# Optimization experiments

Hardware: AMD Instinct MI355X
Metric: run time of the kernel (lower is better)

Reference implementation:

```python
import jax, jax.numpy as jnp
import numpy as np

T = 2048
N = 4096
DT = 0.01
V_RESET = 1.0
ALPHA = 0.01
MAX_SPIKES = 128


def setup_inputs() -> dict:
    key = jax.random.key(0)
    ks = jax.random.split(key, 8)
    ts = jnp.arange(T, dtype=jnp.float32) * DT
    input_current = jax.random.normal(ks[0], (T, N), dtype=jnp.float32)
    # _build_w: uniform(minval=0.5) fully-connected weight matrix
    w = jax.random.uniform(ks[1], (N, N), dtype=jnp.float32, minval=0.5, maxval=1.0)
    # _build_initial: uniform(maxval=0.1)
    v0 = jax.random.uniform(ks[2], (N,), dtype=jnp.float32, maxval=0.1)
    i0 = jax.random.uniform(ks[3], (N,), dtype=jnp.float32, maxval=0.1)
    mu = jax.random.uniform(ks[4], (2,), dtype=jnp.float32, minval=0.5, maxval=1.0)
    # uniforms for initial s and for post-spike s resampling (s = log(u) - alpha)
    s0_u = jax.random.uniform(ks[5], (N,), dtype=jnp.float32)
    resample_u = jax.random.uniform(ks[6], (T, N), dtype=jnp.float32)
    return {"ts": ts, "input_current": input_current, "w": w, "v0": v0,
            "i0": i0, "mu": mu, "s0_u": s0_u, "resample_u": resample_u,
            "max_spikes": MAX_SPIKES}


def reference(ts, input_current, w, v0, i0, mu, s0_u, resample_u, max_spikes):
    """Event-driven spiking net: Euler integration of the drift vf with
    spike events when s crosses 0, followed by the masked per-neuron jump
    transition (_inner_trans_fn) using the firing neuron's weight row.
    Returns trajectory ys [T, N, 3] (v, i, s per neuron)."""
    dt = ts[1] - ts[0]
    eps = jnp.float32(1e-12)
    # s0 = log(uniform) - alpha  (always negative; drifts up at rate intensity(v))
    s0 = jnp.log(s0_u + eps) - ALPHA
    y0 = jnp.stack([v0, i0, s0], axis=-1)  # [N, 3]
    mu1, mu2 = mu[0], mu[1]

    def step(carry, xs):
        y, nsp = carry
        inp_t, ru_t = xs
        v, i, s = y[:, 0], y[:, 1], y[:, 2]
        # drift_vf (Euler step)
        v_n = v + dt * (mu1 * (i - v) + mu1 * inp_t)
        i_n = i + dt * (-mu2 * i)
        s_n = s + dt * jax.nn.sigmoid(v)  # intensity_fn(v)
        # event detection: cond_fn = s; event when s reaches 0
        ev = s_n >= 0.0  # [N] event mask
        fire = jnp.any(ev) & (nsp < max_spikes)
        idx = jnp.argmax(ev)  # event_idx = argmax over event mask
        w_row = w[idx]  # weights from firing neuron to all neurons
        # _inner_trans_fn: spiking neurons reset v and resample s;
        # non-spiking neurons receive current injection w[idx][j]
        v_t = jnp.where(ev, v_n - V_RESET, v_n)
        i_t = jnp.where(ev, i_n, i_n + w_row)
        s_t = jnp.where(ev, jnp.log(ru_t + eps) - ALPHA, s_n)
        y_fire = jnp.stack([v_t, i_t, s_t], axis=-1)
        y_free = jnp.stack([v_n, i_n, s_n], axis=-1)
        y_out = jnp.where(fire, y_fire, y_free)
        nsp = nsp + fire.astype(jnp.int32)
        return (y_out, nsp), y_out

    (_, _), ys = jax.lax.scan(step, (y0, jnp.int32(0)),
                              (input_current, resample_u))
    return ys
```

## Files before the change

### kernel.cpp

```cpp
#include <hip/hip_runtime.h>
#include <stddef.h>

#define TT 2048
#define NN 4096
#define LSEG 64
#define NSEG (TT / LSEG)
#define NBLK 16
#define TPB 256
#define MAXU 0xFFFFFFFFu
#define NOFIRE 0xFFFFFFFEu

__global__ __launch_bounds__(TPB) void phaseA(
    const float* __restrict__ ts, const float* __restrict__ inp,
    const float* __restrict__ w, const float* __restrict__ v0,
    const float* __restrict__ i0, const float* __restrict__ mu,
    const float* __restrict__ s0u, const float* __restrict__ ru,
    const int* __restrict__ mx, float* __restrict__ ys,
    unsigned int* __restrict__ hdr, unsigned int* __restrict__ slots)
{
#pragma clang fp contract(off)
  const int tid = threadIdx.x;
  const int n = blockIdx.x * TPB + tid;
  const float dt = ts[1] - ts[0];
  const float mu1 = mu[0], mu2 = mu[1];
  const int maxs = mx[0];

  float v = v0[n];
  float i_nw = i0[n];
  float s = logf(s0u[n] + 1e-12f) - 0.01f;
  float wv = 0.0f;
  bool applyw = false;
  float inpv = inp[n];
  float ruv  = ru[n];
  int nsp = 0;
  int t_stop = TT;

  __shared__ unsigned int sh_w[TPB / 64];
  __shared__ unsigned int sh_b;

  for (int t = 0; t < TT; ++t) {
    float inpv_n = 0.0f, ruv_n = 0.0f;
    if (t + 1 < TT) {
      inpv_n = inp[(size_t)(t + 1) * NN + n];
      ruv_n  = ru[(size_t)(t + 1) * NN + n];
    }
    float logru = logf(ruv + 1e-12f) - 0.01f;
    float sig = 1.0f / (1.0f + expf(-v));
    float sn = s + dt * sig;
    bool ev = sn >= 0.0f;
    bool coupled = (nsp < maxs);

    if (coupled) {
      unsigned int m = ev ? (unsigned int)n : NOFIRE;
#pragma unroll
      for (int off = 32; off > 0; off >>= 1) {
        unsigned int o = (unsigned int)__shfl_down((int)m, off, 64);
        m = m < o ? m : o;
      }
      if ((tid & 63) == 0) sh_w[tid >> 6] = m;
      __syncthreads();
      if (tid == 0) {
        unsigned int bm = sh_w[0];
        for (int k = 1; k < TPB / 64; ++k) bm = bm < sh_w[k] ? bm : sh_w[k];
        __hip_atomic_store(&slots[(size_t)t * NBLK + blockIdx.x], bm,
                           __ATOMIC_RELAXED, __HIP_MEMORY_SCOPE_AGENT);
      }
    }

    float i_full = applyw ? (i_nw + wv) : i_nw;
    if (t > 0) {
      size_t o = ((size_t)(t - 1) * NN + n) * 3;
      ys[o] = v; ys[o + 1] = i_full; ys[o + 2] = s;
    }
    float vn  = v + dt * (mu1 * (i_full - v) + mu1 * inpv);
    float in_ = i_full + dt * (-mu2 * i_full);

    unsigned int gm = NOFIRE;
    if (coupled) {
      if (tid == 0) {
        unsigned int res = NOFIRE;
        long guard = 0;
        for (;;) {
          unsigned int mn = MAXU;
          bool all = true;
#pragma unroll
          for (int bk = 0; bk < NBLK; ++bk) {
            unsigned int x = __hip_atomic_load(&slots[(size_t)t * NBLK + bk],
                                               __ATOMIC_RELAXED,
                                               __HIP_MEMORY_SCOPE_AGENT);
            all = all && (x != MAXU);
            mn = mn < x ? mn : x;
          }
          if (all || ++guard > (1L << 21)) { res = mn; break; }
        }
        sh_b = res;
      }
      __syncthreads();
      gm = sh_b;
    }

    bool fire = coupled && (gm < (unsigned int)NN);
    applyw = false;
    if (fire) {
      nsp += 1;
      wv = w[(size_t)gm * NN + n];
      if (ev) { v = vn - 1.0f; s = logru; }
      else    { v = vn; s = sn; applyw = true; }
    } else {
      v = vn; s = sn;
    }
    i_nw = in_;
    inpv = inpv_n; ruv = ruv_n;

    if (nsp >= maxs && ((t + 1) & (LSEG - 1)) == 0) { t_stop = t + 1; break; }
  }

  {
    float i_full = applyw ? (i_nw + wv) : i_nw;
    size_t o = ((size_t)(t_stop - 1) * NN + n) * 3;
    ys[o] = v; ys[o + 1] = i_full; ys[o + 2] = s;
  }
  if (n == 0) hdr[0] = (unsigned int)t_stop;
}

__global__ __launch_bounds__(TPB) void p1_segc(
    const float* __restrict__ ts, const float* __restrict__ inp,
    const float* __restrict__ mu, const float* __restrict__ ys,
    const unsigned int* __restrict__ hdr, float* __restrict__ buf1)
{
  unsigned int Kp = hdr[0];
  unsigned int g0 = Kp / LSEG;
  unsigned int g = blockIdx.x >> 4;
  if (g < g0) return;
  int n = (blockIdx.x & 15) * TPB + threadIdx.x;
  float dt = ts[1] - ts[0];
  float mu1 = mu[0], mu2 = mu[1];
  float a = 1.0f - dt * mu1, b = dt * mu1, r = 1.0f - dt * mu2;
  float ibase = ys[((size_t)(Kp - 1) * NN + n) * 3 + 1];
  float ij = ibase * powf(r, (float)((int)(g * LSEG) - (int)Kp));
  float c = 0.0f;
  size_t base = (size_t)(g * LSEG) * NN + n;
  for (int j = 0; j < LSEG; ++j) {
    float x = inp[base + (size_t)j * NN];
    c = a * c + b * (ij + x);
    ij *= r;
  }
  buf1[(size_t)g * NN + n] = c;
}

__global__ __launch_bounds__(TPB) void p2_scanv(
    const float* __restrict__ ts, const float* __restrict__ mu,
    const float* __restrict__ ys, const unsigned int* __restrict__ hdr,
    float* __restrict__ buf1)
{
  unsigned int Kp = hdr[0];
  unsigned int g0 = Kp / LSEG;
  if (g0 >= NSEG) return;
  int n = blockIdx.x * TPB + threadIdx.x;
  float dt = ts[1] - ts[0];
  float mu1 = mu[0];
  float a = 1.0f - dt * mu1;
  float aL = a;
  for (int k = 0; k < 6; ++k) aL *= aL;
  float v = ys[((size_t)(Kp - 1) * NN + n) * 3 + 0];
  for (unsigned int g = g0; g < NSEG; ++g) {
    float cg = buf1[(size_t)g * NN + n];
    buf1[(size_t)g * NN + n] = v;
    v = aL * v + cg;
  }
}

__global__ __launch_bounds__(TPB) void p3_seg(
    const float* __restrict__ ts, const float* __restrict__ inp,
    const float* __restrict__ mu, const unsigned int* __restrict__ hdr,
    const float* __restrict__ buf1, float* __restrict__ buf2,
    float* __restrict__ ys)
{
  unsigned int Kp = hdr[0];
  unsigned int g0 = Kp / LSEG;
  unsigned int g = blockIdx.x >> 4;
  if (g < g0) return;
  int n = (blockIdx.x & 15) * TPB + threadIdx.x;
  float dt = ts[1] - ts[0];
  float mu1 = mu[0], mu2 = mu[1];
  float r = 1.0f - dt * mu2;
  float v = buf1[(size_t)g * NN + n];
  float ibase = ys[((size_t)(Kp - 1) * NN + n) * 3 + 1];
  float i = ibase * powf(r, (float)((int)(g * LSEG) - (int)Kp));
  float sl = 0.0f;
  for (int j = 0; j < LSEG; ++j) {
    size_t t = (size_t)g * LSEG + j;
    float x = inp[t * NN + n];
    float sig = 1.0f / (1.0f + expf(-v));
    sl = sl + dt * sig;
    float vn  = v + dt * (mu1 * (i - v) + mu1 * x);
    float in_ = i + dt * (-mu2 * i);
    size_t o = (t * NN + n) * 3;
    ys[o] = vn; ys[o + 1] = in_; ys[o + 2] = sl;
    v = vn; i = in_;
  }
  buf2[(size_t)g * NN + n] = sl;
}

__global__ __launch_bounds__(TPB) void p4_scans(
    const float* __restrict__ ys, const unsigned int* __restrict__ hdr,
    float* __restrict__ buf2)
{
  unsigned int Kp = hdr[0];
  unsigned int g0 = Kp / LSEG;
  if (g0 >= NSEG) return;
  int n = blockIdx.x * TPB + threadIdx.x;
  float s = ys[((size_t)(Kp - 1) * NN + n) * 3 + 2];
  for (unsigned int g = g0; g < NSEG; ++g) {
    float t = buf2[(size_t)g * NN + n];
    buf2[(size_t)g * NN + n] = s;
    s += t;
  }
}

__global__ __launch_bounds__(TPB) void p5_fixs(
    const unsigned int* __restrict__ hdr, const float* __restrict__ buf2,
    float* __restrict__ ys)
{
  unsigned int Kp = hdr[0];
  size_t e = (size_t)Kp * NN + (size_t)blockIdx.x * TPB + threadIdx.x;
  if (e >= (size_t)TT * NN) return;
  unsigned int t = (unsigned int)(e >> 12);
  unsigned int n = (unsigned int)(e & (NN - 1));
  unsigned int g = t >> 6;
  ys[e * 3 + 2] += buf2[(size_t)g * NN + n];
}

extern "C" void kernel_launch(void* const* d_in, const int* in_sizes, int n_in,
                              void* d_out, int out_size, void* d_ws, size_t ws_size,
                              hipStream_t stream)
{
  (void)in_sizes; (void)n_in; (void)out_size; (void)ws_size;
  const float* ts  = (const float*)d_in[0];
  const float* inp = (const float*)d_in[1];
  const float* w   = (const float*)d_in[2];
  const float* v0  = (const float*)d_in[3];
  const float* i0  = (const float*)d_in[4];
  const float* mu  = (const float*)d_in[5];
  const float* s0u = (const float*)d_in[6];
  const float* ru  = (const float*)d_in[7];
  const int*   mx  = (const int*)d_in[8];
  float* ys = (float*)d_out;

  char* wsb = (char*)d_ws;
  unsigned int* hdr   = (unsigned int*)wsb;
  unsigned int* slots = (unsigned int*)(wsb + 1024);
  float* buf1 = (float*)(wsb + 1024 + (size_t)TT * NBLK * 4);
  float* buf2 = buf1 + (size_t)NSEG * NN;

  hipMemsetAsync(slots, 0xFF, (size_t)TT * NBLK * 4, stream);

  phaseA<<<NBLK, TPB, 0, stream>>>(ts, inp, w, v0, i0, mu, s0u, ru, mx, ys, hdr, slots);
  p1_segc<<<NSEG * 16, TPB, 0, stream>>>(ts, inp, mu, ys, hdr, buf1);
  p2_scanv<<<NN / TPB, TPB, 0, stream>>>(ts, mu, ys, hdr, buf1);
  p3_seg<<<NSEG * 16, TPB, 0, stream>>>(ts, inp, mu, hdr, buf1, buf2, ys);
  p4_scans<<<NN / TPB, TPB, 0, stream>>>(ys, hdr, buf2);
  p5_fixs<<<(TT - 128) * NN / TPB, TPB, 0, stream>>>(hdr, buf2, ys);
}
```

Before: 567.3 us.

## Replicate full neuron state per block to drop inter-block spin sync; fuse s fixup

Phase A no longer splits neurons across blocks that meet through global atomic slots every step. Each of 16 blocks of 1024 threads now simulates all 4096 neurons redundantly, 4 per thread, so the firing argmin comes from an intra-block shuffle and shared-memory reduction. Each block writes only its own quarter-slice of one 256-neuron chunk. The trailing phase also drops the separate s-fixup pass: a sigma-only pass produces segment sums and a final pass recomputes the trajectory and writes ys once with the scanned s offset. The trade is 16x redundant compute and input reads in phase A and one extra recompute pass, in exchange for removing the cross-block spin waits and one read-modify-write sweep of ys.

```diff
diff --git a/kernel.cpp b/kernel.cpp
--- a/kernel.cpp
+++ b/kernel.cpp
@@ -5,122 +5,135 @@
 #define NN 4096
 #define LSEG 64
 #define NSEG (TT / LSEG)
-#define NBLK 16
+#define ABLK 16
+#define ATPB 1024
+#define NPT 4
 #define TPB 256
-#define MAXU 0xFFFFFFFFu
 #define NOFIRE 0xFFFFFFFEu
 
-__global__ __launch_bounds__(TPB) void phaseA(
+__global__ __launch_bounds__(ATPB) void phaseA(
     const float* __restrict__ ts, const float* __restrict__ inp,
     const float* __restrict__ w, const float* __restrict__ v0,
     const float* __restrict__ i0, const float* __restrict__ mu,
     const float* __restrict__ s0u, const float* __restrict__ ru,
     const int* __restrict__ mx, float* __restrict__ ys,
-    unsigned int* __restrict__ hdr, unsigned int* __restrict__ slots)
+    unsigned int* __restrict__ hdr)
 {
 #pragma clang fp contract(off)
   const int tid = threadIdx.x;
-  const int n = blockIdx.x * TPB + tid;
+  const int bid = blockIdx.x;
   const float dt = ts[1] - ts[0];
   const float mu1 = mu[0], mu2 = mu[1];
   const int maxs = mx[0];
 
-  float v = v0[n];
-  float i_nw = i0[n];
-  float s = logf(s0u[n] + 1e-12f) - 0.01f;
-  float wv = 0.0f;
-  bool applyw = false;
-  float inpv = inp[n];
-  float ruv  = ru[n];
-  int nsp = 0;
-  int t_stop = TT;
-
-  __shared__ unsigned int sh_w[TPB / 64];
-  __shared__ unsigned int sh_b;
+  const int kw = bid >> 2;
+  const bool wr = ((tid >> 8) == (bid & 3));
+  const int nw = bid * 256 + (tid & 255);
+
+  float v[NPT], ci[NPT], s[NPT], wv[NPT], inpv[NPT], ruv[NPT];
+  bool aw[NPT];
+#pragma unroll
+  for (int k = 0; k < NPT; ++k) {
+    int n = tid + k * ATPB;
+    v[k] = v0[n];
+    ci[k] = i0[n];
+    s[k] = logf(s0u[n] + 1e-12f) - 0.01f;
+    wv[k] = 0.0f; aw[k] = false;
+    inpv[k] = inp[n];
+    ruv[k]  = ru[n];
+  }
+  int nsp = 0, t_stop = TT;
+
+  __shared__ unsigned int sh_w[2][ATPB / 64];
 
   for (int t = 0; t < TT; ++t) {
-    float inpv_n = 0.0f, ruv_n = 0.0f;
+    float inpn[NPT], run[NPT];
     if (t + 1 < TT) {
-      inpv_n = inp[(size_t)(t + 1) * NN + n];
-      ruv_n  = ru[(size_t)(t + 1) * NN + n];
-    }
-    float logru = logf(ruv + 1e-12f) - 0.01f;
-    float sig = 1.0f / (1.0f + expf(-v));
-    float sn = s + dt * sig;
-    bool ev = sn >= 0.0f;
+#pragma unroll
+      for (int k = 0; k < NPT; ++k) {
+        size_t o = (size_t)(t + 1) * NN + tid + k * ATPB;
+        inpn[k] = inp[o]; run[k] = ru[o];
+      }
+    } else {
+#pragma unroll
+      for (int k = 0; k < NPT; ++k) { inpn[k] = 0.0f; run[k] = 0.0f; }
+    }
+
+    float sn[NPT]; bool ev[NPT];
+    unsigned int m = NOFIRE;
+#pragma unroll
+    for (int k = 0; k < NPT; ++k) {
+      float sig = 1.0f / (1.0f + expf(-v[k]));
+      sn[k] = s[k] + dt * sig;
+      ev[k] = sn[k] >= 0.0f;
+      unsigned int cand = ev[k] ? (unsigned int)(tid + k * ATPB) : NOFIRE;
+      m = m < cand ? m : cand;
+    }
+
     bool coupled = (nsp < maxs);
-
+    unsigned int gm = NOFIRE;
     if (coupled) {
-      unsigned int m = ev ? (unsigned int)n : NOFIRE;
 #pragma unroll
       for (int off = 32; off > 0; off >>= 1) {
         unsigned int o = (unsigned int)__shfl_down((int)m, off, 64);
         m = m < o ? m : o;
       }
-      if ((tid & 63) == 0) sh_w[tid >> 6] = m;
+      if ((tid & 63) == 0) sh_w[t & 1][tid >> 6] = m;
       __syncthreads();
-      if (tid == 0) {
-        unsigned int bm = sh_w[0];
-        for (int k = 1; k < TPB / 64; ++k) bm = bm < sh_w[k] ? bm : sh_w[k];
-        __hip_atomic_store(&slots[(size_t)t * NBLK + blockIdx.x], bm,
-                           __ATOMIC_RELAXED, __HIP_MEMORY_SCOPE_AGENT);
-      }
-    }
-
-    float i_full = applyw ? (i_nw + wv) : i_nw;
-    if (t > 0) {
-      size_t o = ((size_t)(t - 1) * NN + n) * 3;
-      ys[o] = v; ys[o + 1] = i_full; ys[o + 2] = s;
-    }
-    float vn  = v + dt * (mu1 * (i_full - v) + mu1 * inpv);
-    float in_ = i_full + dt * (-mu2 * i_full);
-
-    unsigned int gm = NOFIRE;
-    if (coupled) {
-      if (tid == 0) {
-        unsigned int res = NOFIRE;
-        long guard = 0;
-        for (;;) {
-          unsigned int mn = MAXU;
-          bool all = true;
-#pragma unroll
-          for (int bk = 0; bk < NBLK; ++bk) {
-            unsigned int x = __hip_atomic_load(&slots[(size_t)t * NBLK + bk],
-                                               __ATOMIC_RELAXED,
-                                               __HIP_MEMORY_SCOPE_AGENT);
-            all = all && (x != MAXU);
-            mn = mn < x ? mn : x;
-          }
-          if (all || ++guard > (1L << 21)) { res = mn; break; }
-        }
-        sh_b = res;
-      }
-      __syncthreads();
-      gm = sh_b;
+      unsigned int bm = sh_w[t & 1][0];
+#pragma unroll
+      for (int j = 1; j < ATPB / 64; ++j) {
+        unsigned int x = sh_w[t & 1][j];
+        bm = bm < x ? bm : x;
+      }
+      gm = bm;
+    }
+
+    float fi[NPT];
+#pragma unroll
+    for (int k = 0; k < NPT; ++k) fi[k] = aw[k] ? (ci[k] + wv[k]) : ci[k];
+
+    if (t > 0 && wr) {
+      size_t o = ((size_t)(t - 1) * NN + nw) * 3;
+      ys[o] = v[kw]; ys[o + 1] = fi[kw]; ys[o + 2] = s[kw];
+    }
+
+    float vn[NPT], in_[NPT];
+#pragma unroll
+    for (int k = 0; k < NPT; ++k) {
+      vn[k] = v[k] + dt * (mu1 * (fi[k] - v[k]) + mu1 * inpv[k]);
+      in_[k] = fi[k] + dt * (-mu2 * fi[k]);
     }
 
     bool fire = coupled && (gm < (unsigned int)NN);
-    applyw = false;
+#pragma unroll
+    for (int k = 0; k < NPT; ++k) aw[k] = false;
     if (fire) {
-      nsp += 1;
-      wv = w[(size_t)gm * NN + n];
-      if (ev) { v = vn - 1.0f; s = logru; }
-      else    { v = vn; s = sn; applyw = true; }
+      ++nsp;
+#pragma unroll
+      for (int k = 0; k < NPT; ++k)
+        wv[k] = w[(size_t)gm * NN + tid + k * ATPB];
+#pragma unroll
+      for (int k = 0; k < NPT; ++k) {
+        if (ev[k]) { v[k] = vn[k] - 1.0f; s[k] = logf(ruv[k] + 1e-12f) - 0.01f; }
+        else       { v[k] = vn[k]; s[k] = sn[k]; aw[k] = true; }
+      }
     } else {
-      v = vn; s = sn;
-    }
-    i_nw = in_;
-    inpv = inpv_n; ruv = ruv_n;
+#pragma unroll
+      for (int k = 0; k < NPT; ++k) { v[k] = vn[k]; s[k] = sn[k]; }
+    }
+#pragma unroll
+    for (int k = 0; k < NPT; ++k) { ci[k] = in_[k]; inpv[k] = inpn[k]; ruv[k] = run[k]; }
 
     if (nsp >= maxs && ((t + 1) & (LSEG - 1)) == 0) { t_stop = t + 1; break; }
   }
 
-  {
-    float i_full = applyw ? (i_nw + wv) : i_nw;
-    size_t o = ((size_t)(t_stop - 1) * NN + n) * 3;
-    ys[o] = v; ys[o + 1] = i_full; ys[o + 2] = s;
-  }
-  if (n == 0) hdr[0] = (unsigned int)t_stop;
+  if (wr) {
+    float f = aw[kw] ? (ci[kw] + wv[kw]) : ci[kw];
+    size_t o = ((size_t)(t_stop - 1) * NN + nw) * 3;
+    ys[o] = v[kw]; ys[o + 1] = f; ys[o + 2] = s[kw];
+  }
+  if (bid == 0 && tid == 0) hdr[0] = (unsigned int)t_stop;
 }
 
 __global__ __launch_bounds__(TPB) void p1_segc(
@@ -170,11 +183,11 @@
   }
 }
 
-__global__ __launch_bounds__(TPB) void p3_seg(
+__global__ __launch_bounds__(TPB) void p3a_sigma(
     const float* __restrict__ ts, const float* __restrict__ inp,
     const float* __restrict__ mu, const unsigned int* __restrict__ hdr,
-    const float* __restrict__ buf1, float* __restrict__ buf2,
-    float* __restrict__ ys)
+    const float* __restrict__ buf1, const float* __restrict__ ys,
+    float* __restrict__ buf2)
 {
   unsigned int Kp = hdr[0];
   unsigned int g0 = Kp / LSEG;
@@ -188,15 +201,13 @@
   float ibase = ys[((size_t)(Kp - 1) * NN + n) * 3 + 1];
   float i = ibase * powf(r, (float)((int)(g * LSEG) - (int)Kp));
   float sl = 0.0f;
+  size_t base = (size_t)(g * LSEG) * NN + n;
   for (int j = 0; j < LSEG; ++j) {
-    size_t t = (size_t)g * LSEG + j;
-    float x = inp[t * NN + n];
+    float x = inp[base + (size_t)j * NN];
     float sig = 1.0f / (1.0f + expf(-v));
     sl = sl + dt * sig;
-    float vn  = v + dt * (mu1 * (i - v) + mu1 * x);
+    float vn = v + dt * (mu1 * (i - v) + mu1 * x);
     float in_ = i + dt * (-mu2 * i);
-    size_t o = (t * NN + n) * 3;
-    ys[o] = vn; ys[o + 1] = in_; ys[o + 2] = sl;
     v = vn; i = in_;
   }
   buf2[(size_t)g * NN + n] = sl;
@@ -218,17 +229,35 @@
   }
 }
 
-__global__ __launch_bounds__(TPB) void p5_fixs(
-    const unsigned int* __restrict__ hdr, const float* __restrict__ buf2,
-    float* __restrict__ ys)
-{
-  unsigned int Kp = hdr[0];
-  size_t e = (size_t)Kp * NN + (size_t)blockIdx.x * TPB + threadIdx.x;
-  if (e >= (size_t)TT * NN) return;
-  unsigned int t = (unsigned int)(e >> 12);
-  unsigned int n = (unsigned int)(e & (NN - 1));
-  unsigned int g = t >> 6;
-  ys[e * 3 + 2] += buf2[(size_t)g * NN + n];
+__global__ __launch_bounds__(TPB) void p3b_write(
+    const float* __restrict__ ts, const float* __restrict__ inp,
+    const float* __restrict__ mu, const unsigned int* __restrict__ hdr,
+    const float* __restrict__ buf1, const float* __restrict__ buf2,
+    const float* __restrict__ ysr, float* __restrict__ ys)
+{
+  unsigned int Kp = hdr[0];
+  unsigned int g0 = Kp / LSEG;
+  unsigned int g = blockIdx.x >> 4;
+  if (g < g0) return;
+  int n = (blockIdx.x & 15) * TPB + threadIdx.x;
+  float dt = ts[1] - ts[0];
+  float mu1 = mu[0], mu2 = mu[1];
+  float r = 1.0f - dt * mu2;
+  float v = buf1[(size_t)g * NN + n];
+  float s = buf2[(size_t)g * NN + n];
+  float ibase = ysr[((size_t)(Kp - 1) * NN + n) * 3 + 1];
+  float i = ibase * powf(r, (float)((int)(g * LSEG) - (int)Kp));
+  for (int j = 0; j < LSEG; ++j) {
+    size_t t = (size_t)g * LSEG + j;
+    float x = inp[t * NN + n];
+    float sig = 1.0f / (1.0f + expf(-v));
+    s = s + dt * sig;
+    float vn = v + dt * (mu1 * (i - v) + mu1 * x);
+    float in_ = i + dt * (-mu2 * i);
+    size_t o = (t * NN + n) * 3;
+    ys[o] = vn; ys[o + 1] = in_; ys[o + 2] = s;
+    v = vn; i = in_;
+  }
 }
 
 extern "C" void kernel_launch(void* const* d_in, const int* in_sizes, int n_in,
@@ -248,17 +277,14 @@
   float* ys = (float*)d_out;
 
   char* wsb = (char*)d_ws;
-  unsigned int* hdr   = (unsigned int*)wsb;
-  unsigned int* slots = (unsigned int*)(wsb + 1024);
-  float* buf1 = (float*)(wsb + 1024 + (size_t)TT * NBLK * 4);
+  unsigned int* hdr = (unsigned int*)wsb;
+  float* buf1 = (float*)(wsb + 1024);
   float* buf2 = buf1 + (size_t)NSEG * NN;
 
-  hipMemsetAsync(slots, 0xFF, (size_t)TT * NBLK * 4, stream);
-
-  phaseA<<<NBLK, TPB, 0, stream>>>(ts, inp, w, v0, i0, mu, s0u, ru, mx, ys, hdr, slots);
+  phaseA<<<ABLK, ATPB, 0, stream>>>(ts, inp, w, v0, i0, mu, s0u, ru, mx, ys, hdr);
   p1_segc<<<NSEG * 16, TPB, 0, stream>>>(ts, inp, mu, ys, hdr, buf1);
   p2_scanv<<<NN / TPB, TPB, 0, stream>>>(ts, mu, ys, hdr, buf1);
-  p3_seg<<<NSEG * 16, TPB, 0, stream>>>(ts, inp, mu, hdr, buf1, buf2, ys);
+  p3a_sigma<<<NSEG * 16, TPB, 0, stream>>>(ts, inp, mu, hdr, buf1, ys, buf2);
   p4_scans<<<NN / TPB, TPB, 0, stream>>>(ys, hdr, buf2);
-  p5_fixs<<<(TT - 128) * NN / TPB, TPB, 0, stream>>>(hdr, buf2, ys);
-}
+  p3b_write<<<NSEG * 16, TPB, 0, stream>>>(ts, inp, mu, hdr, buf1, buf2, ys, ys);
+}
```

Result: slower. 595.8 us (+5.0%).
